# Kernel tuning notes

Hardware: AMD Instinct MI355X
Metric: run time of the kernel (lower is better)

The kernel has to match this reference:

```python
import jax, jax.numpy as jnp
from jax import lax
import numpy as np

EPS = 1e-5

def _quant(w):
    # BitNet-style binarization: sign(w) scaled by mean(|w|), with STE (identity grad)
    alpha = jnp.mean(jnp.abs(w))
    wq = jnp.sign(w) * alpha
    return w + lax.stop_gradient(wq - w)

def _bn(x, gamma, beta, axes):
    mean = jnp.mean(x, axis=axes, keepdims=True)
    var = jnp.var(x, axis=axes, keepdims=True)
    shape = [1] * x.ndim
    shape[1] = x.shape[1]
    return (x - mean) * lax.rsqrt(var + EPS) * gamma.reshape(shape) + beta.reshape(shape)

def _conv(x, w):
    return lax.conv_general_dilated(x, w, window_strides=(1, 1), padding=((1, 1), (1, 1)),
                                    dimension_numbers=('NCHW', 'OIHW', 'NCHW'))

def _maxpool2(x):
    return lax.reduce_window(x, -jnp.inf, lax.max, (1, 1, 2, 2), (1, 1, 2, 2), 'VALID')

def setup_inputs() -> dict:
    key = jax.random.key(0)
    ks = jax.random.split(key, 5)
    return {
        'x': jax.random.normal(ks[0], (1024, 3, 32, 32), jnp.float32),
        'w1': jax.random.normal(ks[1], (64, 3, 3, 3), jnp.float32) * 0.1,
        'g1': jnp.ones((64,), jnp.float32), 'b1': jnp.zeros((64,), jnp.float32),
        'w2': jax.random.normal(ks[2], (128, 64, 3, 3), jnp.float32) * 0.05,
        'g2': jnp.ones((128,), jnp.float32), 'b2': jnp.zeros((128,), jnp.float32),
        'wfc1': jax.random.normal(ks[3], (256, 8192), jnp.float32) * 0.02,
        'g3': jnp.ones((256,), jnp.float32), 'b3': jnp.zeros((256,), jnp.float32),
        'wfc2': jax.random.normal(ks[4], (10, 256), jnp.float32) * 0.1,
    }

def reference(x, w1, g1, b1, w2, g2, b2, wfc1, g3, b3, wfc2):
    h = _conv(x, _quant(w1))                 # [B,64,32,32]
    h = _maxpool2(jax.nn.relu(_bn(h, g1, b1, (0, 2, 3))))  # [B,64,16,16]
    h = _conv(h, _quant(w2))                 # [B,128,16,16]
    h = _maxpool2(jax.nn.relu(_bn(h, g2, b2, (0, 2, 3))))  # [B,128,8,8]
    h = h.reshape(h.shape[0], -1)            # [B,8192]
    h = h @ _quant(wfc1).T                   # [B,256]
    h = jax.nn.relu(_bn(h, g3, b3, (0,)))
    return h @ _quant(wfc2).T                # [B,10]
```

## Files before the change

kernel.cpp:

```cpp
#include <hip/hip_runtime.h>
#include <stdint.h>

typedef unsigned short u16;
typedef unsigned int u32;
typedef __attribute__((ext_vector_type(8))) short s8v;
typedef __attribute__((ext_vector_type(4))) float f4v;
typedef __attribute__((ext_vector_type(8))) u16 u16x8;
typedef __attribute__((ext_vector_type(4))) u16 u16x4;

__device__ __forceinline__ float bf2f(u16 u){
  union { u32 i; float f; } v; v.i = ((u32)u) << 16; return v.f;
}
__device__ __forceinline__ u16 f2bf(float f){
  union { float f; u32 i; } v; v.f = f;
  u32 i = v.i;
  return (u16)((i + 0x7fffu + ((i >> 16) & 1u)) >> 16);
}
__device__ __forceinline__ float sgnf(float w){
  return (w > 0.f) ? 1.f : ((w < 0.f) ? -1.f : 0.f);
}
__device__ __forceinline__ u16 sgn_bf(float w){
  return (w > 0.f) ? (u16)0x3F80 : ((w < 0.f) ? (u16)0xBF80 : (u16)0);
}

#define GLL16(gaddr, laddr) __builtin_amdgcn_global_load_lds( \
    (const __attribute__((address_space(1))) void*)(gaddr),   \
    (__attribute__((address_space(3))) void*)(laddr), 16, 0, 0)


__global__ __launch_bounds__(256) void k_gen(const float* __restrict__ w1, const float* __restrict__ w2,
                                             const float* __restrict__ wfc2, const float* __restrict__ wfc1,
                                             u16* __restrict__ qw1b, u16* __restrict__ qw2b,
                                             float* __restrict__ qwfc2, u16* __restrict__ qfc1b,
                                             float* __restrict__ partials){
  __shared__ u16 tile[128*72];
  int t = threadIdx.x;
  if (blockIdx.x < 306){
    int i = blockIdx.x * 256 + t;
    float av = 0.f; int slot;
    if (i < 73728){
      int j = i & 7, lane = (i >> 3) & 63, fid = i >> 9;
      int s = fid >> 4, ks = (fid >> 3) & 1, nt = fid & 7;
      int co = (lane & 15)*8 + nt;
      int c_pos = ks*32 + (lane >> 4)*8 + j;
      int c6 = c_pos & 63;
      int c_orig = ((c6 & 3) << 4) + (c6 >> 2);
      float wv = w2[((size_t)co*64 + c_orig)*9 + s];
      qw2b[i] = sgn_bf(wv);
      av = fabsf(wv); slot = 1;
    } else if (i < 73728 + 2048){
      int i3 = i - 73728;
      int j = i3 & 7, lane = (i3 >> 3) & 63, nt = i3 >> 9;
      int co = nt*16 + (lane & 15);
      int k = (lane >> 4)*8 + j;
      if (k < 27){
        float wv = w1[co*27 + k];
        qw1b[i3] = sgn_bf(wv);
        av = fabsf(wv);
      } else qw1b[i3] = (u16)0;
      slot = 0;
    } else {
      int i4 = i - (73728 + 2048);
      float wv = wfc2[i4];
      qwfc2[i4] = sgnf(wv);
      av = fabsf(wv); slot = 3;
    }
    #pragma unroll
    for (int off = 32; off > 0; off >>= 1) av += __shfl_xor(av, off);
    if ((t & 63) == 0) atomicAdd(partials + slot*256 + (blockIdx.x & 255), av);
  } else {
    int co = blockIdx.x - 306;
    const float4* src = (const float4*)(wfc1 + (size_t)co*8192);
    float av = 0.f;
    #pragma unroll
    for (int p = 0; p < 8; ++p){
      int k4 = t + p*256;
      float4 v = src[k4];
      int c = k4 >> 4, px = (k4 & 15)*4;
      u16* d = tile + c*72 + px;
      d[0] = sgn_bf(v.x); d[1] = sgn_bf(v.y); d[2] = sgn_bf(v.z); d[3] = sgn_bf(v.w);
      av += fabsf(v.x) + fabsf(v.y) + fabsf(v.z) + fabsf(v.w);
    }
    #pragma unroll
    for (int off = 32; off > 0; off >>= 1) av += __shfl_xor(av, off);
    if ((t & 63) == 0) atomicAdd(partials + 2*256 + (co & 255), av);
    __syncthreads();
    int co4 = co >> 4, co15 = co & 15;
    #pragma unroll
    for (int p = 0; p < 4; ++p){
      int m = t + p*256;
      int px = m >> 4, jj = m & 15;
      int kstep = px*4 + (jj >> 2), l16 = jj & 3;
      u16x8 o;
      #pragma unroll
      for (int u = 0; u < 8; ++u) o[u] = tile[(jj*8 + u)*72 + px];
      *(u16x8*)(qfc1b + ((size_t)(kstep*16 + co4)*512 + (l16*16 + co15)*8)) = o;
    }
  }
}

__global__ void k_red4(const float* __restrict__ partials, float* __restrict__ absum){
  int t = threadIdx.x, w = t >> 6, lane = t & 63;
  const float* p = partials + w*256;
  float s = p[lane] + p[lane + 64] + p[lane + 128] + p[lane + 192];
  #pragma unroll
  for (int off = 32; off > 0; off >>= 1) s += __shfl_xor(s, off);
  if (lane == 0) absum[w] = s;
}

__global__ __launch_bounds__(256) void k_conv1m(const float* __restrict__ x, const u16* __restrict__ qw1b,
                                                const float* __restrict__ absum, u16* __restrict__ p1raw,
                                                float* __restrict__ gs, float* __restrict__ gq){
  __shared__ __align__(8) u16 xs[3*34*36];
  __shared__ float ls1[64], ls2[64];
  int n = blockIdx.x, t = threadIdx.x;
  if (t < 64){ ls1[t] = 0.f; ls2[t] = 0.f; }
  for (int i = t; i < 1836; i += 256) ((u32*)xs)[i] = 0u;
  __syncthreads();
  const float4* xg = (const float4*)(x + (size_t)n * 3072);
  for (int i = t; i < 768; i += 256){
    float4 v = xg[i];
    int ci = i >> 8, rem = i & 255, y = rem >> 3, xq = (rem & 7) * 4;
    int base = ci*1224 + (y+1)*36 + 2 + xq;
    *(u32*)(xs + base)     = (u32)f2bf(v.x) | ((u32)f2bf(v.y) << 16);
    *(u32*)(xs + base + 2) = (u32)f2bf(v.z) | ((u32)f2bf(v.w) << 16);
  }
  int w = t >> 6, lane = t & 63, l15 = lane & 15, q = lane >> 4;
  int koff[8]; u32 kmsk[8];
  #pragma unroll
  for (int j = 0; j < 8; ++j){
    int k = q*8 + j;
    int d9 = (k*57) >> 9;
    int r9 = k - d9*9;
    int d3 = (r9*11) >> 5;
    int r3 = r9 - d3*3;
    koff[j] = d9*1224 + d3*36 + r3;
    kmsk[j] = (k < 27) ? 0xffffu : 0u;
  }
  const s8v* bp = (const s8v*)qw1b;
  s8v bf[4];
  #pragma unroll
  for (int nt = 0; nt < 4; ++nt) bf[nt] = bp[nt*64 + lane];
  float alpha = absum[0] * (1.f/1728.f);
  u16* p1img = p1raw + (size_t)n * 16384;
  float s1v[4], s2v[4];
  #pragma unroll
  for (int nt = 0; nt < 4; ++nt){ s1v[nt] = 0.f; s2v[nt] = 0.f; }
  __syncthreads();
  for (int chunk = 0; chunk < 4; ++chunk){
    #pragma unroll
    for (int i = 0; i < 4; ++i){
      int tl = w*4 + i;
      int r = tl*16 + l15;
      int g = (chunk*256 + r) >> 2, s = r & 3;
      int iy = 2*(g >> 4) + (s >> 1), ix = 2*(g & 15) + (s & 1);
      const u16* xb = xs + iy*36 + ix + 1;
      u32 pk2[4];
      #pragma unroll
      for (int kk = 0; kk < 4; ++kk){
        u32 lo = (u32)xb[koff[2*kk]]     & kmsk[2*kk];
        u32 hi = (u32)xb[koff[2*kk + 1]] & kmsk[2*kk + 1];
        pk2[kk] = lo | (hi << 16);
      }
      s8v av;
      ((u32*)&av)[0] = pk2[0]; ((u32*)&av)[1] = pk2[1];
      ((u32*)&av)[2] = pk2[2]; ((u32*)&av)[3] = pk2[3];
      int go = chunk*64 + tl*4 + q;
      u16x4 pk;
      #pragma unroll
      for (int nt = 0; nt < 4; ++nt){
        f4v c = (f4v)(0.0f);
        c = __builtin_amdgcn_mfma_f32_16x16x32_bf16(av, bf[nt], c, 0, 0, 0);
        s1v[nt] += c[0] + c[1] + c[2] + c[3];
        s2v[nt] += c[0]*c[0] + c[1]*c[1] + c[2]*c[2] + c[3]*c[3];
        float pm = fmaxf(fmaxf(c[0], c[1]), fmaxf(c[2], c[3]));
        pk[nt] = f2bf(pm * alpha);
      }
      *(u16x4*)(p1img + go*64 + l15*4) = pk;
    }
  }
  #pragma unroll
  for (int nt = 0; nt < 4; ++nt){
    s1v[nt] += __shfl_xor(s1v[nt], 16); s1v[nt] += __shfl_xor(s1v[nt], 32);
    s2v[nt] += __shfl_xor(s2v[nt], 16); s2v[nt] += __shfl_xor(s2v[nt], 32);
  }
  if (q == 0){
    #pragma unroll
    for (int nt = 0; nt < 4; ++nt){
      atomicAdd(&ls1[l15*4 + nt], s1v[nt]);
      atomicAdd(&ls2[l15*4 + nt], s2v[nt]);
    }
  }
  __syncthreads();
  if (t < 64){
    atomicAdd(gs + t, ls1[t] * alpha);
    atomicAdd(gq + t, ls2[t] * alpha * alpha);
  }
}

__global__ __launch_bounds__(512, 4) void k_conv2m(const u16* __restrict__ p1raw, const u16* __restrict__ qw2b,
                                                   const float* __restrict__ absum,
                                                   const float* __restrict__ s1, const float* __restrict__ q1,
                                                   const float* __restrict__ g1, const float* __restrict__ b1,
                                                   u16* __restrict__ p2raw,
                                                   float* __restrict__ gs, float* __restrict__ gq, int n0){
  __shared__ __align__(16) u16 img[288*64];
  __shared__ __align__(16) u16 bstage[3][4096];
  int n = blockIdx.x + n0, t = threadIdx.x;
  int c0 = (t & 7) * 8;
  float scv[8], biv[8];
  #pragma unroll
  for (int j = 0; j < 8; ++j){
    int cp = c0 + j;
    int corig = ((cp & 3) << 4) + (cp >> 2);
    float m = s1[cp] * (1.f/1048576.f);
    float var = q1[cp] * (1.f/1048576.f) - m*m;
    float sc = g1[corig] * rsqrtf(var + 1e-5f);
    scv[j] = sc; biv[j] = b1[corig] - m*sc;
  }
  if (t < 256){
    int cl = t >> 7, y = (t >> 3) & 15, unit = t & 7;
    int px = y*18 + cl*17;
    int su = unit ^ (px & 7);
    *(u16x8*)(img + px*64 + su*8) = (u16x8)(u16)0;
  }
  const u16* src = p1raw + (size_t)n * 16384;
  #pragma unroll
  for (int i = 0; i < 4; ++i){
    int id = i*512 + t;
    int p0 = id >> 3, unit = id & 7;
    int y = p0 >> 4, xq = p0 & 15;
    int px = y*18 + xq + 1;
    int su = unit ^ (px & 7);
    u16x8 v = *(const u16x8*)(src + id*8);
    u16x8 o;
    #pragma unroll
    for (int j = 0; j < 8; ++j)
      o[j] = f2bf(fmaxf(bf2f(v[j]) * scv[j] + biv[j], 0.f));
    *(u16x8*)(img + px*64 + su*8) = o;
  }
  int w = t >> 6, lane = t & 63, l15 = lane & 15, q = lane >> 4;
  int wr = w >> 1, wc = w & 1;
  const char* bsrc = (const char*)qw2b;
  {
    const char* g = bsrc + w*1024 + lane*16;
    GLL16(g, ((char*)bstage[0]) + w*1024);
  }
  __syncthreads();
  f4v acc[4][4];
  #pragma unroll
  for (int a = 0; a < 4; ++a)
    #pragma unroll
    for (int b = 0; b < 4; ++b) acc[a][b] = (f4v)(0.0f);
  for (int p = 0; p < 18; ++p){
    int s = p >> 1, ks = p & 1;
    int dy = s / 3, dx = s - dy*3;
    if (p < 17){
      const char* g = bsrc + (size_t)(p + 1)*8192 + w*1024 + lane*16;
      GLL16(g, ((char*)bstage[(p + 1) % 3]) + w*1024);
      asm volatile("s_waitcnt vmcnt(1)" ::: "memory");
    } else {
      asm volatile("s_waitcnt vmcnt(0)" ::: "memory");
    }
    __builtin_amdgcn_s_barrier();
    asm volatile("" ::: "memory");
    const u16* bb = bstage[p % 3];
    s8v bf[4];
    #pragma unroll
    for (int nt = 0; nt < 4; ++nt) bf[nt] = *(const s8v*)(bb + ((wc*4 + nt)*64 + lane)*8);
    __builtin_amdgcn_s_setprio(1);
    #pragma unroll
    for (int mt = 0; mt < 4; ++mt){
      int yv = wr*4 + mt + dy - 1;
      if (yv >= 0 && yv <= 15){
        int px = yv*18 + l15 + dx;
        int su = (ks*4 + q) ^ (px & 7);
        s8v av = *(const s8v*)(img + px*64 + su*8);
        #pragma unroll
        for (int nt = 0; nt < 4; ++nt)
          acc[mt][nt] = __builtin_amdgcn_mfma_f32_16x16x32_bf16(av, bf[nt], acc[mt][nt], 0, 0, 0);
      }
    }
    __builtin_amdgcn_s_setprio(0);
  }
  float alpha = absum[1] * (1.f/73728.f);
  float s1v[4], s2v[4];
  #pragma unroll
  for (int nt = 0; nt < 4; ++nt){ s1v[nt] = 0.f; s2v[nt] = 0.f; }
  #pragma unroll
  for (int mp = 0; mp < 2; ++mp){
    #pragma unroll
    for (int rp = 0; rp < 2; ++rp){
      u16x4 pk;
      #pragma unroll
      for (int nt = 0; nt < 4; ++nt){
        float v0 = acc[2*mp][nt][2*rp]     * alpha;
        float v1 = acc[2*mp][nt][2*rp+1]   * alpha;
        float v2 = acc[2*mp+1][nt][2*rp]   * alpha;
        float v3 = acc[2*mp+1][nt][2*rp+1] * alpha;
        s1v[nt] += v0 + v1 + v2 + v3;
        s2v[nt] += v0*v0 + v1*v1 + v2*v2 + v3*v3;
        pk[nt] = f2bf(fmaxf(fmaxf(v0, v1), fmaxf(v2, v3)));
      }
      int opx = (wr*2 + mp)*8 + (q*2 + rp);
      *(u16x4*)(p2raw + ((size_t)n*64 + opx)*128 + l15*8 + wc*4) = pk;
    }
  }
  #pragma unroll
  for (int nt = 0; nt < 4; ++nt){
    s1v[nt] += __shfl_xor(s1v[nt], 16); s1v[nt] += __shfl_xor(s1v[nt], 32);
    s2v[nt] += __shfl_xor(s2v[nt], 16); s2v[nt] += __shfl_xor(s2v[nt], 32);
  }
  __syncthreads();
  float* ls = (float*)img;
  if (t < 256) ls[t] = 0.f;
  __syncthreads();
  if (q == 0){
    #pragma unroll
    for (int nt = 0; nt < 4; ++nt){
      atomicAdd(&ls[l15*8 + wc*4 + nt], s1v[nt]);
      atomicAdd(&ls[128 + l15*8 + wc*4 + nt], s2v[nt]);
    }
  }
  __syncthreads();
  if (t < 128){ atomicAdd(gs + t, ls[t]); atomicAdd(gq + t, ls[128 + t]); }
}

__global__ __launch_bounds__(256) void k_fc1m(const u16* __restrict__ p2, const u16* __restrict__ qfc1b,
                                              const float* __restrict__ absum,
                                              const float* __restrict__ s2, const float* __restrict__ q2,
                                              const float* __restrict__ g2, const float* __restrict__ b2,
                                              float* __restrict__ h3p){
  int t = threadIdx.x;
  int bm = blockIdx.x, bn = blockIdx.y, kb = blockIdx.z;
  int w = t >> 6, lane = t & 63, l15 = lane & 15, q = lane >> 4;
  int wr = w >> 1, wc = w & 1;
  int rowbase = bm*32 + wr*16;
  int ntb = bn*8 + wc*4;
  const s8v* bp = (const s8v*)qfc1b;
  f4v acc[4];
  #pragma unroll
  for (int b = 0; b < 4; ++b) acc[b] = (f4v)(0.0f);
  #pragma unroll
  for (int ks4 = 0; ks4 < 4; ++ks4){
    int c0 = ks4*32 + q*8;
    float scv[8], biv[8];
    #pragma unroll
    for (int j = 0; j < 8; ++j){
      float m = s2[c0+j] * (1.f/262144.f);
      float var = q2[c0+j] * (1.f/262144.f) - m*m;
      float sc = g2[c0+j] * rsqrtf(var + 1e-5f);
      scv[j] = sc; biv[j] = b2[c0+j] - m*sc;
    }
    #pragma unroll 2
    for (int u = 0; u < 8; ++u){
      int ks = ks4 + u*4;
      int kst = kb*32 + ks;
      s8v bf[4];
      #pragma unroll
      for (int nt = 0; nt < 4; ++nt) bf[nt] = bp[(kst*16 + ntb + nt)*64 + lane];
      u16x8 araw = *(const u16x8*)(p2 + (size_t)(rowbase + l15)*8192 + kst*32 + q*8);
      s8v av;
      #pragma unroll
      for (int j = 0; j < 8; ++j){
        float f = fmaxf(bf2f(araw[j]) * scv[j] + biv[j], 0.f);
        ((u16*)&av)[j] = f2bf(f);
      }
      #pragma unroll
      for (int nt = 0; nt < 4; ++nt)
        acc[nt] = __builtin_amdgcn_mfma_f32_16x16x32_bf16(av, bf[nt], acc[nt], 0, 0, 0);
    }
  }
  float alpha = absum[2] * (1.f/2097152.f);
  float* dst = h3p + (size_t)kb * 262144;
  #pragma unroll
  for (int nt = 0; nt < 4; ++nt){
    int col = (ntb + nt)*16 + l15;
    #pragma unroll
    for (int r = 0; r < 4; ++r)
      dst[(size_t)(rowbase + q*4 + r)*256 + col] = acc[nt][r] * alpha;
  }
}

__global__ __launch_bounds__(256) void k_fin3f(const float* __restrict__ h3p, float* __restrict__ h3,
                                               float* __restrict__ s3, float* __restrict__ q3){
  int jb = blockIdx.x, ns = blockIdx.y, t = threadIdx.x;
  int jj = t & 31, nn = t >> 5;
  int j = jb*32 + jj;
  float s1 = 0.f, s2 = 0.f;
  #pragma unroll
  for (int i = 0; i < 2; ++i){
    int n = ns*16 + i*8 + nn;
    float v = 0.f;
    #pragma unroll
    for (int kb = 0; kb < 8; ++kb) v += h3p[(size_t)kb*262144 + n*256 + j];
    h3[n*256 + j] = v;
    s1 += v; s2 += v*v;
  }
  __shared__ float l1[256], l2[256];
  l1[t] = s1; l2[t] = s2;
  __syncthreads();
  if (t < 32){
    float a = 0.f, b = 0.f;
    #pragma unroll
    for (int k = 0; k < 8; ++k){ a += l1[t+32*k]; b += l2[t+32*k]; }
    atomicAdd(s3 + jb*32 + t, a); atomicAdd(q3 + jb*32 + t, b);
  }
}

__global__ __launch_bounds__(64) void k_fc2(const float* __restrict__ h3, const float* __restrict__ qwfc2,
                                            const float* __restrict__ absum,
                                            const float* __restrict__ s3, const float* __restrict__ q3,
                                            const float* __restrict__ g3, const float* __restrict__ b3,
                                            float* __restrict__ out){
  int n = blockIdx.x, lane = threadIdx.x;
  float a[4];
  #pragma unroll
  for (int i = 0; i < 4; ++i){
    int j = lane + 64*i;
    float m = s3[j] * (1.f/1024.f);
    float var = q3[j] * (1.f/1024.f) - m*m;
    float sc = g3[j] * rsqrtf(var + 1e-5f);
    float v = h3[(size_t)n*256 + j] * sc + (b3[j] - m*sc);
    a[i] = fmaxf(v, 0.f);
  }
  float alpha = absum[3] * (1.f/2560.f);
  #pragma unroll
  for (int k = 0; k < 10; ++k){
    float p = 0.f;
    #pragma unroll
    for (int i = 0; i < 4; ++i) p += a[i] * qwfc2[k*256 + lane + 64*i];
    #pragma unroll
    for (int off = 32; off > 0; off >>= 1) p += __shfl_down(p, off);
    if (lane == 0) out[n*10 + k] = p * alpha;
  }
}

extern "C" void kernel_launch(void* const* d_in, const int* in_sizes, int n_in,
                              void* d_out, int out_size, void* d_ws, size_t ws_size,
                              hipStream_t stream){
  (void)in_sizes; (void)n_in; (void)out_size; (void)ws_size;
  const float* x    = (const float*)d_in[0];
  const float* w1   = (const float*)d_in[1];
  const float* g1   = (const float*)d_in[2];
  const float* b1   = (const float*)d_in[3];
  const float* w2   = (const float*)d_in[4];
  const float* g2   = (const float*)d_in[5];
  const float* b2   = (const float*)d_in[6];
  const float* wfc1 = (const float*)d_in[7];
  const float* g3   = (const float*)d_in[8];
  const float* b3   = (const float*)d_in[9];
  const float* wfc2 = (const float*)d_in[10];
  float* out = (float*)d_out;

  float* wsf = (float*)d_ws;
  char*  wsb = (char*)d_ws;
  float* absum = wsf;
  float* s1 = wsf + 16;   float* q1 = wsf + 80;
  float* s2 = wsf + 144;  float* q2 = wsf + 272;
  float* s3 = wsf + 1024; float* q3 = wsf + 1280;
  float* partials = wsf + 2048;
  u16*   qw1b  = (u16*)(wsf + 4096);
  u16*   qw2b  = (u16*)(wsb + (64u << 10));
  float* qwfc2 = (float*)(wsb + (256u << 10));
  float* h3    = (float*)(wsb + (1ull << 20));
  u16*   qfc1b = (u16*)(wsb + (2ull << 20));
  u16*   p1t   = (u16*)(wsb + (8ull << 20) + 4096);
  u16*   p2    = (u16*)(wsb + (112ull << 20));
  float* h3p   = (float*)(wsb + (128ull << 20));

  hipMemsetAsync(wsf, 0, 3072 * sizeof(float), stream);
  k_gen<<<562, 256, 0, stream>>>(w1, w2, wfc2, wfc1, qw1b, qw2b, qwfc2, qfc1b, partials);
  k_red4<<<1, 256, 0, stream>>>(partials, absum);
  k_conv1m<<<1024, 256, 0, stream>>>(x, qw1b, absum, p1t, s1, q1);
  k_conv2m<<<512, 512, 0, stream>>>(p1t, qw2b, absum, s1, q1, g1, b1, p2, s2, q2, 0);
  k_conv2m<<<512, 512, 0, stream>>>(p1t, qw2b, absum, s1, q1, g1, b1, p2, s2, q2, 512);
  k_fc1m<<<dim3(32, 2, 8), 256, 0, stream>>>(p2, qfc1b, absum, s2, q2, g2, b2, h3p);
  k_fin3f<<<dim3(8, 64), 256, 0, stream>>>(h3p, h3, s3, q3);
  k_fc2<<<1024, 64, 0, stream>>>(h3, qwfc2, absum, s3, q3, g3, b3, out);
}
```

Before: 218.8 us.

## Drop weight-scale alphas absorbed by batch norm, remove reduction kernel, merge conv2 launches

```diff
diff --git a/kernel.cpp b/kernel.cpp
--- a/kernel.cpp
+++ b/kernel.cpp
@@ -32,12 +32,11 @@
                                              const float* __restrict__ wfc2, const float* __restrict__ wfc1,
                                              u16* __restrict__ qw1b, u16* __restrict__ qw2b,
                                              float* __restrict__ qwfc2, u16* __restrict__ qfc1b,
-                                             float* __restrict__ partials){
+                                             float* __restrict__ absum){
   __shared__ u16 tile[128*72];
   int t = threadIdx.x;
   if (blockIdx.x < 306){
     int i = blockIdx.x * 256 + t;
-    float av = 0.f; int slot;
     if (i < 73728){
       int j = i & 7, lane = (i >> 3) & 63, fid = i >> 9;
       int s = fid >> 4, ks = (fid >> 3) & 1, nt = fid & 7;
@@ -45,33 +44,25 @@
       int c_pos = ks*32 + (lane >> 4)*8 + j;
       int c6 = c_pos & 63;
       int c_orig = ((c6 & 3) << 4) + (c6 >> 2);
-      float wv = w2[((size_t)co*64 + c_orig)*9 + s];
-      qw2b[i] = sgn_bf(wv);
-      av = fabsf(wv); slot = 1;
+      qw2b[i] = sgn_bf(w2[((size_t)co*64 + c_orig)*9 + s]);
     } else if (i < 73728 + 2048){
       int i3 = i - 73728;
       int j = i3 & 7, lane = (i3 >> 3) & 63, nt = i3 >> 9;
       int co = nt*16 + (lane & 15);
       int k = (lane >> 4)*8 + j;
-      if (k < 27){
-        float wv = w1[co*27 + k];
-        qw1b[i3] = sgn_bf(wv);
-        av = fabsf(wv);
-      } else qw1b[i3] = (u16)0;
-      slot = 0;
+      qw1b[i3] = (k < 27) ? sgn_bf(w1[co*27 + k]) : (u16)0;
     } else {
       int i4 = i - (73728 + 2048);
       float wv = wfc2[i4];
       qwfc2[i4] = sgnf(wv);
-      av = fabsf(wv); slot = 3;
-    }
-    #pragma unroll
-    for (int off = 32; off > 0; off >>= 1) av += __shfl_xor(av, off);
-    if ((t & 63) == 0) atomicAdd(partials + slot*256 + (blockIdx.x & 255), av);
+      float av = fabsf(wv);
+      #pragma unroll
+      for (int off = 32; off > 0; off >>= 1) av += __shfl_xor(av, off);
+      if ((t & 63) == 0) atomicAdd(absum + 3, av);
+    }
   } else {
     int co = blockIdx.x - 306;
     const float4* src = (const float4*)(wfc1 + (size_t)co*8192);
-    float av = 0.f;
     #pragma unroll
     for (int p = 0; p < 8; ++p){
       int k4 = t + p*256;
@@ -79,11 +70,7 @@
       int c = k4 >> 4, px = (k4 & 15)*4;
       u16* d = tile + c*72 + px;
       d[0] = sgn_bf(v.x); d[1] = sgn_bf(v.y); d[2] = sgn_bf(v.z); d[3] = sgn_bf(v.w);
-      av += fabsf(v.x) + fabsf(v.y) + fabsf(v.z) + fabsf(v.w);
-    }
-    #pragma unroll
-    for (int off = 32; off > 0; off >>= 1) av += __shfl_xor(av, off);
-    if ((t & 63) == 0) atomicAdd(partials + 2*256 + (co & 255), av);
+    }
     __syncthreads();
     int co4 = co >> 4, co15 = co & 15;
     #pragma unroll
@@ -99,17 +86,8 @@
   }
 }
 
-__global__ void k_red4(const float* __restrict__ partials, float* __restrict__ absum){
-  int t = threadIdx.x, w = t >> 6, lane = t & 63;
-  const float* p = partials + w*256;
-  float s = p[lane] + p[lane + 64] + p[lane + 128] + p[lane + 192];
-  #pragma unroll
-  for (int off = 32; off > 0; off >>= 1) s += __shfl_xor(s, off);
-  if (lane == 0) absum[w] = s;
-}
-
 __global__ __launch_bounds__(256) void k_conv1m(const float* __restrict__ x, const u16* __restrict__ qw1b,
-                                                const float* __restrict__ absum, u16* __restrict__ p1raw,
+                                                u16* __restrict__ p1raw,
                                                 float* __restrict__ gs, float* __restrict__ gq){
   __shared__ __align__(8) u16 xs[3*34*36];
   __shared__ float ls1[64], ls2[64];
@@ -141,7 +119,6 @@
   s8v bf[4];
   #pragma unroll
   for (int nt = 0; nt < 4; ++nt) bf[nt] = bp[nt*64 + lane];
-  float alpha = absum[0] * (1.f/1728.f);
   u16* p1img = p1raw + (size_t)n * 16384;
   float s1v[4], s2v[4];
   #pragma unroll
@@ -174,7 +151,7 @@
         s1v[nt] += c[0] + c[1] + c[2] + c[3];
         s2v[nt] += c[0]*c[0] + c[1]*c[1] + c[2]*c[2] + c[3]*c[3];
         float pm = fmaxf(fmaxf(c[0], c[1]), fmaxf(c[2], c[3]));
-        pk[nt] = f2bf(pm * alpha);
+        pk[nt] = f2bf(pm);
       }
       *(u16x4*)(p1img + go*64 + l15*4) = pk;
     }
@@ -193,20 +170,19 @@
   }
   __syncthreads();
   if (t < 64){
-    atomicAdd(gs + t, ls1[t] * alpha);
-    atomicAdd(gq + t, ls2[t] * alpha * alpha);
+    atomicAdd(gs + t, ls1[t]);
+    atomicAdd(gq + t, ls2[t]);
   }
 }
 
 __global__ __launch_bounds__(512, 4) void k_conv2m(const u16* __restrict__ p1raw, const u16* __restrict__ qw2b,
-                                                   const float* __restrict__ absum,
                                                    const float* __restrict__ s1, const float* __restrict__ q1,
                                                    const float* __restrict__ g1, const float* __restrict__ b1,
                                                    u16* __restrict__ p2raw,
-                                                   float* __restrict__ gs, float* __restrict__ gq, int n0){
+                                                   float* __restrict__ gs, float* __restrict__ gq){
   __shared__ __align__(16) u16 img[288*64];
   __shared__ __align__(16) u16 bstage[3][4096];
-  int n = blockIdx.x + n0, t = threadIdx.x;
+  int n = blockIdx.x, t = threadIdx.x;
   int c0 = (t & 7) * 8;
   float scv[8], biv[8];
   #pragma unroll
@@ -283,7 +259,6 @@
     }
     __builtin_amdgcn_s_setprio(0);
   }
-  float alpha = absum[1] * (1.f/73728.f);
   float s1v[4], s2v[4];
   #pragma unroll
   for (int nt = 0; nt < 4; ++nt){ s1v[nt] = 0.f; s2v[nt] = 0.f; }
@@ -294,10 +269,10 @@
       u16x4 pk;
       #pragma unroll
       for (int nt = 0; nt < 4; ++nt){
-        float v0 = acc[2*mp][nt][2*rp]     * alpha;
-        float v1 = acc[2*mp][nt][2*rp+1]   * alpha;
-        float v2 = acc[2*mp+1][nt][2*rp]   * alpha;
-        float v3 = acc[2*mp+1][nt][2*rp+1] * alpha;
+        float v0 = acc[2*mp][nt][2*rp];
+        float v1 = acc[2*mp][nt][2*rp+1];
+        float v2 = acc[2*mp+1][nt][2*rp];
+        float v3 = acc[2*mp+1][nt][2*rp+1];
         s1v[nt] += v0 + v1 + v2 + v3;
         s2v[nt] += v0*v0 + v1*v1 + v2*v2 + v3*v3;
         pk[nt] = f2bf(fmaxf(fmaxf(v0, v1), fmaxf(v2, v3)));
@@ -327,7 +302,6 @@
 }
 
 __global__ __launch_bounds__(256) void k_fc1m(const u16* __restrict__ p2, const u16* __restrict__ qfc1b,
-                                              const float* __restrict__ absum,
                                               const float* __restrict__ s2, const float* __restrict__ q2,
                                               const float* __restrict__ g2, const float* __restrict__ b2,
                                               float* __restrict__ h3p){
@@ -371,14 +345,13 @@
         acc[nt] = __builtin_amdgcn_mfma_f32_16x16x32_bf16(av, bf[nt], acc[nt], 0, 0, 0);
     }
   }
-  float alpha = absum[2] * (1.f/2097152.f);
   float* dst = h3p + (size_t)kb * 262144;
   #pragma unroll
   for (int nt = 0; nt < 4; ++nt){
     int col = (ntb + nt)*16 + l15;
     #pragma unroll
     for (int r = 0; r < 4; ++r)
-      dst[(size_t)(rowbase + q*4 + r)*256 + col] = acc[nt][r] * alpha;
+      dst[(size_t)(rowbase + q*4 + r)*256 + col] = acc[nt][r];
   }
 }
 
@@ -408,12 +381,13 @@
   }
 }
 
-__global__ __launch_bounds__(64) void k_fc2(const float* __restrict__ h3, const float* __restrict__ qwfc2,
-                                            const float* __restrict__ absum,
-                                            const float* __restrict__ s3, const float* __restrict__ q3,
-                                            const float* __restrict__ g3, const float* __restrict__ b3,
-                                            float* __restrict__ out){
-  int n = blockIdx.x, lane = threadIdx.x;
+__global__ __launch_bounds__(256) void k_fc2(const float* __restrict__ h3, const float* __restrict__ qwfc2,
+                                             const float* __restrict__ absum,
+                                             const float* __restrict__ s3, const float* __restrict__ q3,
+                                             const float* __restrict__ g3, const float* __restrict__ b3,
+                                             float* __restrict__ out){
+  int t = threadIdx.x;
+  int n = blockIdx.x*4 + (t >> 6), lane = t & 63;
   float a[4];
   #pragma unroll
   for (int i = 0; i < 4; ++i){
@@ -459,7 +433,6 @@
   float* s1 = wsf + 16;   float* q1 = wsf + 80;
   float* s2 = wsf + 144;  float* q2 = wsf + 272;
   float* s3 = wsf + 1024; float* q3 = wsf + 1280;
-  float* partials = wsf + 2048;
   u16*   qw1b  = (u16*)(wsf + 4096);
   u16*   qw2b  = (u16*)(wsb + (64u << 10));
   float* qwfc2 = (float*)(wsb + (256u << 10));
@@ -469,13 +442,11 @@
   u16*   p2    = (u16*)(wsb + (112ull << 20));
   float* h3p   = (float*)(wsb + (128ull << 20));
 
-  hipMemsetAsync(wsf, 0, 3072 * sizeof(float), stream);
-  k_gen<<<562, 256, 0, stream>>>(w1, w2, wfc2, wfc1, qw1b, qw2b, qwfc2, qfc1b, partials);
-  k_red4<<<1, 256, 0, stream>>>(partials, absum);
-  k_conv1m<<<1024, 256, 0, stream>>>(x, qw1b, absum, p1t, s1, q1);
-  k_conv2m<<<512, 512, 0, stream>>>(p1t, qw2b, absum, s1, q1, g1, b1, p2, s2, q2, 0);
-  k_conv2m<<<512, 512, 0, stream>>>(p1t, qw2b, absum, s1, q1, g1, b1, p2, s2, q2, 512);
-  k_fc1m<<<dim3(32, 2, 8), 256, 0, stream>>>(p2, qfc1b, absum, s2, q2, g2, b2, h3p);
+  hipMemsetAsync(wsf, 0, 2048 * sizeof(float), stream);
+  k_gen<<<562, 256, 0, stream>>>(w1, w2, wfc2, wfc1, qw1b, qw2b, qwfc2, qfc1b, absum);
+  k_conv1m<<<1024, 256, 0, stream>>>(x, qw1b, p1t, s1, q1);
+  k_conv2m<<<1024, 512, 0, stream>>>(p1t, qw2b, s1, q1, g1, b1, p2, s2, q2);
+  k_fc1m<<<dim3(32, 2, 8), 256, 0, stream>>>(p2, qfc1b, s2, q2, g2, b2, h3p);
   k_fin3f<<<dim3(8, 64), 256, 0, stream>>>(h3p, h3, s3, q3);
-  k_fc2<<<1024, 64, 0, stream>>>(h3, qwfc2, absum, s3, q3, g3, b3, out);
-}
+  k_fc2<<<256, 256, 0, stream>>>(h3, qwfc2, absum, s3, q3, g3, b3, out);
+}
```

After: 213.6 us. 2.4% less time.
